# Kernel optimization log

Measured on AMD Instinct MI355X. Metric: run time of the kernel, lower is better.

Reference implementation:

```python
import jax, jax.numpy as jnp
import numpy as np
from jax import lax

# sRGB linear -> LMS matrix (Oklab M1)
M1 = jnp.array([[0.4122214708, 0.5363325363, 0.0514459929],
                [0.2119034982, 0.6806995451, 0.1073969566],
                [0.0883024619, 0.2817188376, 0.6299787005]], dtype=jnp.float32)
# LMS^(1/3) -> Oklab matrix (Oklab M2)
M2 = jnp.array([[0.2104542553, 0.7936177850, -0.0040720468],
                [1.9779984951, -2.4285922050, 0.4505937099],
                [0.0259040371, 0.7827717662, -0.8086757660]], dtype=jnp.float32)
_SX = jnp.array([[-1., 0., 1.], [-2., 0., 2.], [-1., 0., 1.]], dtype=jnp.float32)
_SY = jnp.array([[-1., -2., -1.], [0., 0., 0.], [1., 2., 1.]], dtype=jnp.float32)
SOBEL = jnp.stack([_SX, _SY])[:, None]  # (2,1,3,3) cross-correlation kernels

CLOSING_KERNEL = 11
CLOSING_PAD = CLOSING_KERNEL // 2
EDGE_THRESHOLD = 0.5
POST_DILATION = 2
EPS = 0.01


def _srgb_to_linear(srgb):
    srgb = jnp.clip(srgb, 0.0, 1.0)
    return jnp.where(srgb <= 0.04045, srgb / 12.92, ((srgb + 0.055) / 1.055) ** 2.4)


def _rgb_to_oklab(rgb):  # [B,3,H,W] -> [B,3,H,W]
    linear = _srgb_to_linear(rgb)
    lms = jnp.einsum('oc,bchw->bohw', M1, linear)
    lms = jnp.clip(lms, 1e-10, None) ** (1.0 / 3.0)
    return jnp.einsum('oc,bchw->bohw', M2, lms)


def _max_pool(x, k, p):  # torch max_pool2d pads with -inf implicitly
    return lax.reduce_window(x, -jnp.inf, lax.max, (1, 1, k, k), (1, 1, 1, 1),
                             [(0, 0), (0, 0), (p, p), (p, p)])


def _min_pool(x, k, p):  # -max_pool(-x): padding becomes +inf
    return lax.reduce_window(x, jnp.inf, lax.min, (1, 1, k, k), (1, 1, 1, 1),
                             [(0, 0), (0, 0), (p, p), (p, p)])


def _omni_edge(img):  # [B,C,H,W] -> [B,1,H,W]
    B, C, H, W = img.shape
    flat = img.reshape(B * C, 1, H, W)
    g = lax.conv_general_dilated(flat, SOBEL, (1, 1), [(1, 1), (1, 1)])  # [B*C,2,H,W]
    grad = (jnp.abs(g[:, 0]) + jnp.abs(g[:, 1])).reshape(B, C, H, W)
    return jnp.max(grad, axis=1, keepdims=True)


def _crevice_mask(target):
    edge_soft = jnp.clip(_omni_edge(target) / EDGE_THRESHOLD, 0.0, 1.0)
    dilated = _max_pool(edge_soft, CLOSING_KERNEL, CLOSING_PAD)
    closed = _min_pool(dilated, CLOSING_KERNEL, CLOSING_PAD)
    mask = jax.nn.relu(closed - edge_soft)
    if POST_DILATION > 0:
        dk = 2 * POST_DILATION + 1
        mask = _max_pool(mask, dk, POST_DILATION)
    return mask


def setup_inputs() -> dict:
    key = jax.random.key(0)
    k1, k2 = jax.random.split(key)
    shape = (8, 3, 1024, 1024)
    pred = jax.random.uniform(k1, shape, dtype=jnp.float32)
    target = jax.random.uniform(k2, shape, dtype=jnp.float32)
    return {"pred": pred, "target": target}


def reference(pred, target):
    crevice_mask = _crevice_mask(target)
    mask_sum = jnp.maximum(crevice_mask.sum(), 1.0)
    pred_lab = _rgb_to_oklab(pred)
    target_lab = _rgb_to_oklab(target)
    p_a, p_b = pred_lab[:, 1:2], pred_lab[:, 2:3]
    t_a, t_b = target_lab[:, 1:2], target_lab[:, 2:3]
    C_pred = jnp.sqrt(p_a ** 2 + p_b ** 2 + 1e-12)
    C_gt = jnp.sqrt(t_a ** 2 + t_b ** 2 + 1e-12)
    chroma_loss = (jnp.abs(C_pred - C_gt) * crevice_mask).sum() / mask_sum
    dot_ab = p_a * t_a + p_b * t_b
    cos_hue_diff = jnp.clip(dot_ab / (C_pred * C_gt + 1e-12), -1.0, 1.0)
    hue_loss = (jnp.clip(C_gt, EPS, None) * (1.0 - cos_hue_diff) * crevice_mask).sum() / mask_sum
    return chroma_loss + 2.0 * hue_loss
```

## Files before the change

kernel.cpp:

```cpp
#include <hip/hip_runtime.h>
#include <math.h>

#define SROWS 64
#define PCH   16
#define QCAP  1024


__device__ __forceinline__ float srgb_to_linear(float x) {
    x = fminf(fmaxf(x, 0.0f), 1.0f);
    return (x <= 0.04045f) ? x * (1.0f / 12.92f)
                           : powf((x + 0.055f) * (1.0f / 1.055f), 2.4f);
}

__device__ __forceinline__ void oklab_ab(float r, float g, float b,
                                         float& A, float& Bc) {
    r = srgb_to_linear(r);
    g = srgb_to_linear(g);
    b = srgb_to_linear(b);
    float l = 0.4122214708f * r + 0.5363325363f * g + 0.0514459929f * b;
    float m = 0.2119034982f * r + 0.6806995451f * g + 0.1073969566f * b;
    float s = 0.0883024619f * r + 0.2817188376f * g + 0.6299787005f * b;
    l = cbrtf(fmaxf(l, 1e-10f));
    m = cbrtf(fmaxf(m, 1e-10f));
    s = cbrtf(fmaxf(s, 1e-10f));
    A  = 1.9779984951f * l - 2.428592205f * m + 0.4505937099f * s;
    Bc = 0.0259040371f * l + 0.7827717662f * m - 0.808675766f  * s;
}

__device__ __forceinline__ void color_terms(const float* __restrict__ pred,
                                            const float* __restrict__ target,
                                            size_t off, size_t HWp, float m,
                                            float& sc, float& sh) {
    float pa, pb, ta, tb;
    oklab_ab(pred[off], pred[off + HWp], pred[off + 2 * HWp], pa, pb);
    oklab_ab(target[off], target[off + HWp], target[off + 2 * HWp], ta, tb);
    float Cp = sqrtf(pa * pa + pb * pb + 1e-12f);
    float Cg = sqrtf(ta * ta + tb * tb + 1e-12f);
    sc += fabsf(Cp - Cg) * m;
    float cosd = (pa * ta + pb * tb) / (Cp * Cg + 1e-12f);
    cosd = fminf(fmaxf(cosd, -1.0f), 1.0f);
    sh += fmaxf(Cg, 0.01f) * (1.0f - cosd) * m;
}


__global__ __launch_bounds__(256) void k1_edge(const float* __restrict__ target,
                                               float* __restrict__ edge,
                                               int H, int W) {
    const int WC = 62, BC = 248;
    int cb = (W + BC - 1) / BC;
    int rs = H / SROWS;
    int blk = blockIdx.x;
    int b   = blk / (cb * rs);
    int t   = blk % (cb * rs);
    int bxi = t / rs, ysi = t % rs;
    int lane = threadIdx.x & 63, wid = threadIdx.x >> 6;
    int c  = bxi * BC + wid * WC + lane - 1;
    int y0 = ysi * SROWS;
    size_t plane = (size_t)H * W;
    const float* tb = target + (size_t)b * 3 * plane;
    bool inc = (c >= 0 && c < W);
    bool store_ok = (lane >= 1 && lane <= WC && c < W);
    float* ep = edge + (size_t)b * plane + c;
    int lp = min(lane + 1, 63), lm = max(lane - 1, 0);

    float pr0, pr1, pr2, cu0, cu1, cu2;
    {
        bool ok = inc && (y0 - 1 >= 0);
        const float* p = tb + (size_t)(y0 - 1) * W + c;
        pr0 = ok ? p[0] : 0.f; pr1 = ok ? p[plane] : 0.f; pr2 = ok ? p[2 * plane] : 0.f;
    }
    {
        const float* p = tb + (size_t)y0 * W + c;
        cu0 = inc ? p[0] : 0.f; cu1 = inc ? p[plane] : 0.f; cu2 = inc ? p[2 * plane] : 0.f;
    }
#pragma unroll 2
    for (int y = y0; y < y0 + SROWS; ++y) {
        bool ok = inc && (y + 1 < H);
        const float* p = tb + (size_t)(y + 1) * W + c;
        float nx0 = ok ? p[0] : 0.f;
        float nx1 = ok ? p[plane] : 0.f;
        float nx2 = ok ? p[2 * plane] : 0.f;
        float g = 0.f;
#define SOBEL_CH(PR, CU, NX)                                              \
        {                                                                 \
            float u = PR + 2.f * CU + NX;                                 \
            float v = NX - PR;                                            \
            float up = __shfl(u, lp), um = __shfl(u, lm);                 \
            float vp = __shfl(v, lp), vm = __shfl(v, lm);                 \
            g = fmaxf(g, fabsf(up - um) + fabsf(vm + 2.f * v + vp));      \
        }
        SOBEL_CH(pr0, cu0, nx0)
        SOBEL_CH(pr1, cu1, nx1)
        SOBEL_CH(pr2, cu2, nx2)
#undef SOBEL_CH
        if (store_ok) ep[(size_t)y * W] = fminf(2.f * g, 1.f);
        pr0 = cu0; pr1 = cu1; pr2 = cu2;
        cu0 = nx0; cu1 = nx1; cu2 = nx2;
    }
}


template <int R, bool ISMAX, bool SUB_EDGE>
__global__ __launch_bounds__(256) void pool_kernel(const float* __restrict__ in,
                                                   const float* __restrict__ edge,
                                                   float* __restrict__ out,
                                                   int H, int W) {
    const int OUTW = 256 - 2 * R;
    __shared__ float s_v[PCH][256];
    int cb = (W + OUTW - 1) / OUTW;
    int rs = H / SROWS;
    int blk = blockIdx.x;
    int b   = blk / (cb * rs);
    int t   = blk % (cb * rs);
    int bxi = t / rs, ysi = t % rs;
    int tid = threadIdx.x;
    int col = bxi * OUTW - R + tid;
    int cc  = min(max(col, 0), W - 1);
    size_t base = (size_t)b * H * W;
    const float* colp = in + base + cc;
    int ys = ysi * SROWS;
    bool writer = (tid >= R) && (tid < OUTW + R) && (col < W);

    for (int ph = 0; ph < SROWS / PCH; ++ph) {
        int y0 = ys + ph * PCH;
        float w[PCH + 2 * R];
#pragma unroll
        for (int k = 0; k < PCH + 2 * R; ++k) {
            int r = min(max(y0 - R + k, 0), H - 1);
            w[k] = colp[(size_t)r * W];
        }
        float v[PCH];
#pragma unroll
        for (int k = 0; k < PCH; ++k) {
            float m = w[k];
#pragma unroll
            for (int d = 1; d <= 2 * R; ++d)
                m = ISMAX ? fmaxf(m, w[k + d]) : fminf(m, w[k + d]);
            v[k] = m;
        }
        __syncthreads();
#pragma unroll
        for (int k = 0; k < PCH; ++k) s_v[k][tid] = v[k];
        __syncthreads();
        if (writer) {
#pragma unroll
            for (int k = 0; k < PCH; ++k) {
                float m = s_v[k][tid - R];
#pragma unroll
                for (int d = 1; d <= 2 * R; ++d)
                    m = ISMAX ? fmaxf(m, s_v[k][tid - R + d])
                              : fminf(m, s_v[k][tid - R + d]);
                size_t gi = base + (size_t)(y0 + k) * W + col;
                out[gi] = SUB_EDGE ? fmaxf(m - edge[gi], 0.f) : m;
            }
        }
    }
}


__global__ __launch_bounds__(256) void k4_loss(const float* __restrict__ pred,
                                               const float* __restrict__ target,
                                               const float* __restrict__ mask0,
                                               float* __restrict__ partials,
                                               int H, int W, int nb) {
    const int R = 2, OUTW = 256 - 2 * R;
    __shared__ float s_v[PCH][256];
    __shared__ int   q_pos[QCAP];
    __shared__ float q_m[QCAP];
    __shared__ int   cnt;
    __shared__ float s_red[3][4];

    int cb = (W + OUTW - 1) / OUTW;
    int rs = H / SROWS;
    int blk = blockIdx.x;
    int b   = blk / (cb * rs);
    int t   = blk % (cb * rs);
    int bxi = t / rs, ysi = t % rs;
    int tid = threadIdx.x;
    int col = bxi * OUTW - R + tid;
    int cc  = min(max(col, 0), W - 1);
    size_t HWp  = (size_t)H * W;
    size_t base = (size_t)b * HWp;
    size_t cbase = (size_t)b * 3 * HWp;
    const float* colp = mask0 + base + cc;
    int ys = ysi * SROWS;
    bool writer = (tid >= R) && (tid < OUTW + R) && (col < W);

    float sm = 0.f, sc = 0.f, sh = 0.f;

    for (int ph = 0; ph < SROWS / PCH; ++ph) {
        int y0 = ys + ph * PCH;
        float w[PCH + 2 * R];
#pragma unroll
        for (int k = 0; k < PCH + 2 * R; ++k) {
            int r = min(max(y0 - R + k, 0), H - 1);
            w[k] = colp[(size_t)r * W];
        }
        float v[PCH];
#pragma unroll
        for (int k = 0; k < PCH; ++k) {
            float m = w[k];
#pragma unroll
            for (int d = 1; d <= 2 * R; ++d) m = fmaxf(m, w[k + d]);
            v[k] = m;
        }
        __syncthreads();
#pragma unroll
        for (int k = 0; k < PCH; ++k) s_v[k][tid] = v[k];
        if (tid == 0) cnt = 0;
        __syncthreads();
        if (writer) {
#pragma unroll
            for (int k = 0; k < PCH; ++k) {
                float m = s_v[k][tid - R];
#pragma unroll
                for (int d = 1; d <= 2 * R; ++d)
                    m = fmaxf(m, s_v[k][tid - R + d]);
                sm += m;
                if (m > 0.f) {
                    int pos = atomicAdd(&cnt, 1);
                    if (pos < QCAP) {
                        q_pos[pos] = ((y0 + k) << 16) | col;
                        q_m[pos] = m;
                    } else {
                        color_terms(pred, target,
                                    cbase + (size_t)(y0 + k) * W + col,
                                    HWp, m, sc, sh);
                    }
                }
            }
        }
        __syncthreads();
        int n = min(cnt, QCAP);
        for (int i = tid; i < n; i += 256) {
            int pk = q_pos[i];
            color_terms(pred, target,
                        cbase + (size_t)(pk >> 16) * W + (pk & 0xffff),
                        HWp, q_m[i], sc, sh);
        }
    }

#pragma unroll
    for (int off = 32; off > 0; off >>= 1) {
        sm += __shfl_down(sm, off);
        sc += __shfl_down(sc, off);
        sh += __shfl_down(sh, off);
    }
    int lane = tid & 63, wav = tid >> 6;
    __syncthreads();
    if (lane == 0) { s_red[0][wav] = sm; s_red[1][wav] = sc; s_red[2][wav] = sh; }
    __syncthreads();
    if (tid == 0) {
        float tm = 0, tc = 0, th = 0;
        for (int i = 0; i < 4; ++i) {
            tm += s_red[0][i]; tc += s_red[1][i]; th += s_red[2][i];
        }
        partials[blk]          = tm;
        partials[nb + blk]     = tc;
        partials[2 * nb + blk] = th;
    }
}

__global__ void finalize_kernel(const float* __restrict__ partials, int nb,
                                float* __restrict__ out) {
    double sm = 0.0, sc = 0.0, sh = 0.0;
    for (int i = threadIdx.x; i < nb; i += blockDim.x) {
        sm += (double)partials[i];
        sc += (double)partials[nb + i];
        sh += (double)partials[2 * nb + i];
    }
    __shared__ double red[3][256];
    red[0][threadIdx.x] = sm;
    red[1][threadIdx.x] = sc;
    red[2][threadIdx.x] = sh;
    __syncthreads();
    for (int s = blockDim.x / 2; s > 0; s >>= 1) {
        if ((int)threadIdx.x < s) {
            red[0][threadIdx.x] += red[0][threadIdx.x + s];
            red[1][threadIdx.x] += red[1][threadIdx.x + s];
            red[2][threadIdx.x] += red[2][threadIdx.x + s];
        }
        __syncthreads();
    }
    if (threadIdx.x == 0) {
        double ms = fmax(red[0][0], 1.0);
        out[0] = (float)(red[1][0] / ms + 2.0 * red[2][0] / ms);
    }
}


extern "C" void kernel_launch(void* const* d_in, const int* in_sizes, int n_in,
                              void* d_out, int out_size, void* d_ws, size_t ws_size,
                              hipStream_t stream) {
    const float* pred   = (const float*)d_in[0];
    const float* target = (const float*)d_in[1];
    float* out = (float*)d_out;

    const int H = 1024, W = 1024;
    int Bn = in_sizes[0] / (3 * H * W);
    size_t plane = (size_t)Bn * H * W * sizeof(float);

    char* ws = (char*)d_ws;
    float* planeA = (float*)ws;
    float* planeB = (float*)(ws + plane);
    float* partials = (float*)(ws + 2 * plane);

    int rs = H / SROWS;
    int cb1 = (W + 247) / 248;
    int cbP = (W + 245) / 246;
    int cb4 = (W + 251) / 252;
    int g1 = Bn * cb1 * rs;
    int gP = Bn * cbP * rs;
    int g4 = Bn * cb4 * rs;

    k1_edge<<<g1, 256, 0, stream>>>(target, planeA, H, W);
    pool_kernel<5, true, false><<<gP, 256, 0, stream>>>(planeA, nullptr, planeB, H, W);
    pool_kernel<5, false, true><<<gP, 256, 0, stream>>>(planeB, planeA, planeA, H, W);
    k4_loss<<<g4, 256, 0, stream>>>(pred, target, planeA, partials, H, W, g4);
    finalize_kernel<<<1, 256, 0, stream>>>(partials, g4, out);
}
```

Baseline: 109.7 us.

## Fuse Sobel edge kernel with 11x11 max-pool dilation into one kernel

Merges the edge-detection kernel and the first max-pool pass into a single kernel that computes Sobel edges for 16-row chunks plus a 5-row halo, then does vertical and horizontal max-dilation through shared memory. It writes both the edge plane and the dilated plane, removing one full-plane write/read round trip and a kernel launch. In exchange it recomputes edges in halo rows and columns, which adds redundant Sobel work, uses more shared memory and registers (a 28-value window per thread), and adds extra barriers per chunk.

New measurement: 266.2 us. 2.43x slower.

```diff
diff --git a/kernel.cpp b/kernel.cpp
--- a/kernel.cpp
+++ b/kernel.cpp
@@ -4,6 +4,7 @@
 #define SROWS 64
 #define PCH   16
 #define QCAP  1024
+#define OUTW12 244
 
 
 __device__ __forceinline__ float srgb_to_linear(float x) {
@@ -43,59 +44,117 @@
 }
 
 
-__global__ __launch_bounds__(256) void k1_edge(const float* __restrict__ target,
-                                               float* __restrict__ edge,
-                                               int H, int W) {
-    const int WC = 62, BC = 248;
-    int cb = (W + BC - 1) / BC;
-    int rs = H / SROWS;
+__global__ __launch_bounds__(256) void k12_fused(const float* __restrict__ target,
+                                                 float* __restrict__ edge,
+                                                 float* __restrict__ dil,
+                                                 int H, int W) {
+    __shared__ float s_u[26][256];
+    __shared__ float s_v[26][256];
+    float (*s_dv)[256] = s_u;
+
+    int cgs = (W + OUTW12 - 1) / OUTW12;
+    int rs  = H / SROWS;
     int blk = blockIdx.x;
-    int b   = blk / (cb * rs);
-    int t   = blk % (cb * rs);
-    int bxi = t / rs, ysi = t % rs;
-    int lane = threadIdx.x & 63, wid = threadIdx.x >> 6;
-    int c  = bxi * BC + wid * WC + lane - 1;
-    int y0 = ysi * SROWS;
-    size_t plane = (size_t)H * W;
-    const float* tb = target + (size_t)b * 3 * plane;
-    bool inc = (c >= 0 && c < W);
-    bool store_ok = (lane >= 1 && lane <= WC && c < W);
-    float* ep = edge + (size_t)b * plane + c;
-    int lp = min(lane + 1, 63), lm = max(lane - 1, 0);
-
-    float pr0, pr1, pr2, cu0, cu1, cu2;
-    {
-        bool ok = inc && (y0 - 1 >= 0);
-        const float* p = tb + (size_t)(y0 - 1) * W + c;
-        pr0 = ok ? p[0] : 0.f; pr1 = ok ? p[plane] : 0.f; pr2 = ok ? p[2 * plane] : 0.f;
-    }
-    {
-        const float* p = tb + (size_t)y0 * W + c;
-        cu0 = inc ? p[0] : 0.f; cu1 = inc ? p[plane] : 0.f; cu2 = inc ? p[2 * plane] : 0.f;
-    }
-#pragma unroll 2
-    for (int y = y0; y < y0 + SROWS; ++y) {
-        bool ok = inc && (y + 1 < H);
-        const float* p = tb + (size_t)(y + 1) * W + c;
-        float nx0 = ok ? p[0] : 0.f;
-        float nx1 = ok ? p[plane] : 0.f;
-        float nx2 = ok ? p[2 * plane] : 0.f;
-        float g = 0.f;
-#define SOBEL_CH(PR, CU, NX)                                              \
-        {                                                                 \
-            float u = PR + 2.f * CU + NX;                                 \
-            float v = NX - PR;                                            \
-            float up = __shfl(u, lp), um = __shfl(u, lm);                 \
-            float vp = __shfl(v, lp), vm = __shfl(v, lm);                 \
-            g = fmaxf(g, fabsf(up - um) + fabsf(vm + 2.f * v + vp));      \
-        }
-        SOBEL_CH(pr0, cu0, nx0)
-        SOBEL_CH(pr1, cu1, nx1)
-        SOBEL_CH(pr2, cu2, nx2)
-#undef SOBEL_CH
-        if (store_ok) ep[(size_t)y * W] = fminf(2.f * g, 1.f);
-        pr0 = cu0; pr1 = cu1; pr2 = cu2;
-        cu0 = nx0; cu1 = nx1; cu2 = nx2;
+    int b   = blk / (cgs * rs);
+    int rem = blk % (cgs * rs);
+    int bxi = rem / rs, ysi = rem % rs;
+    int t   = threadIdx.x;
+    int c0  = bxi * OUTW12;
+    int gcol = c0 - 6 + t;
+    int scc  = min(max(gcol, 0), W - 1);
+    bool colok = (gcol >= 0) && (gcol < W);
+    size_t HW = (size_t)H * W;
+    const float* tb = target + (size_t)b * 3 * HW + scc;
+    size_t obase = (size_t)b * HW;
+    int ys = ysi * SROWS;
+    int tl = max(t - 1, 0), tr = min(t + 1, 255);
+
+    int gc2 = min(max(gcol, 0), W - 1);
+    int tc  = gc2 - (c0 - 6);
+    bool needfix = (gcol != gc2);
+
+    bool dil_store  = (t < OUTW12) && (c0 + t < W);
+    bool edge_store = (t >= 6) && (t < 6 + OUTW12) && (gcol < W);
+
+    for (int ph = 0; ph < SROWS / PCH; ++ph) {
+        int f0 = ys + ph * PCH;
+        float e[26];
+#pragma unroll
+        for (int i = 0; i < 26; ++i) e[i] = 0.f;
+
+        for (int c = 0; c < 3; ++c) {
+            const float* p = tb + (size_t)c * HW;
+            float w[28];
+#pragma unroll
+            for (int i = 0; i < 28; ++i) {
+                int r  = f0 - 6 + i;
+                int rc = min(max(r, 0), H - 1);
+                float val = p[(size_t)rc * W];
+                w[i] = (colok && r >= 0 && r < H) ? val : 0.f;
+            }
+            float u[26], v[26];
+#pragma unroll
+            for (int i = 0; i < 26; ++i) {
+                u[i] = fmaf(2.f, w[i + 1], w[i]) + w[i + 2];
+                v[i] = w[i + 2] - w[i];
+            }
+            __syncthreads();
+#pragma unroll
+            for (int i = 0; i < 26; ++i) {
+                s_u[i][t] = u[i];
+                s_v[i][t] = v[i];
+            }
+            __syncthreads();
+#pragma unroll
+            for (int i = 0; i < 26; ++i) {
+                float ul = s_u[i][tl], ur = s_u[i][tr];
+                float vl = s_v[i][tl], vr = s_v[i][tr];
+                float gx = ur - ul;
+                float gy = fmaf(2.f, v[i], vl) + vr;
+                e[i] = fmaxf(e[i], fabsf(gx) + fabsf(gy));
+            }
+        }
+#pragma unroll
+        for (int i = 0; i < 26; ++i) e[i] = fminf(2.f * e[i], 1.f);
+        if (f0 == 0) {
+            e[0] = e[5]; e[1] = e[5]; e[2] = e[5]; e[3] = e[5]; e[4] = e[5];
+        }
+        if (f0 == H - PCH) {
+            e[21] = e[20]; e[22] = e[20]; e[23] = e[20]; e[24] = e[20];
+            e[25] = e[20];
+        }
+        float dv[16];
+#pragma unroll
+        for (int m = 0; m < 16; m += 2) {
+            float M = e[m + 1];
+#pragma unroll
+            for (int d = 2; d <= 10; ++d) M = fmaxf(M, e[m + d]);
+            dv[m]     = fmaxf(M, e[m]);
+            dv[m + 1] = fmaxf(M, e[m + 11]);
+        }
+        __syncthreads();
+#pragma unroll
+        for (int k = 0; k < 16; ++k) s_dv[k][t] = dv[k];
+        __syncthreads();
+        if (needfix) {
+#pragma unroll
+            for (int k = 0; k < 16; ++k) s_dv[k][t] = s_dv[k][tc];
+        }
+        __syncthreads();
+        if (dil_store) {
+#pragma unroll
+            for (int k = 0; k < 16; ++k) {
+                float m = s_dv[k][t + 1];
+#pragma unroll
+                for (int d = 2; d <= 11; ++d) m = fmaxf(m, s_dv[k][t + d]);
+                dil[obase + (size_t)(f0 + k) * W + (c0 + t)] = m;
+            }
+        }
+        if (edge_store) {
+#pragma unroll
+            for (int k = 0; k < 16; ++k)
+                edge[obase + (size_t)(f0 + k) * W + gcol] = e[5 + k];
+        }
     }
 }
 
@@ -251,12 +310,12 @@
     if (lane == 0) { s_red[0][wav] = sm; s_red[1][wav] = sc; s_red[2][wav] = sh; }
     __syncthreads();
     if (tid == 0) {
-        float tm = 0, tc = 0, th = 0;
+        float tm = 0, tc2 = 0, th = 0;
         for (int i = 0; i < 4; ++i) {
-            tm += s_red[0][i]; tc += s_red[1][i]; th += s_red[2][i];
+            tm += s_red[0][i]; tc2 += s_red[1][i]; th += s_red[2][i];
         }
         partials[blk]          = tm;
-        partials[nb + blk]     = tc;
+        partials[nb + blk]     = tc2;
         partials[2 * nb + blk] = th;
     }
 }
@@ -305,16 +364,15 @@
     float* planeB = (float*)(ws + plane);
     float* partials = (float*)(ws + 2 * plane);
 
-    int rs = H / SROWS;
-    int cb1 = (W + 247) / 248;
+    int rs  = H / SROWS;
+    int cgs = (W + OUTW12 - 1) / OUTW12;
+    int g12 = Bn * cgs * rs;
     int cbP = (W + 245) / 246;
     int cb4 = (W + 251) / 252;
-    int g1 = Bn * cb1 * rs;
     int gP = Bn * cbP * rs;
     int g4 = Bn * cb4 * rs;
 
-    k1_edge<<<g1, 256, 0, stream>>>(target, planeA, H, W);
-    pool_kernel<5, true, false><<<gP, 256, 0, stream>>>(planeA, nullptr, planeB, H, W);
+    k12_fused<<<g12, 256, 0, stream>>>(target, planeA, planeB, H, W);
     pool_kernel<5, false, true><<<gP, 256, 0, stream>>>(planeB, planeA, planeA, H, W);
     k4_loss<<<g4, 256, 0, stream>>>(pred, target, planeA, partials, H, W, g4);
     finalize_kernel<<<1, 256, 0, stream>>>(partials, g4, out);
```

## Rewrite Sobel edge kernel with LDS row chunks instead of wavefront shuffles

Applied to the files above, without the earlier changes.

The edge kernel changes from per-wavefront column strips with a rolling three-row register window and lane shuffles to 256-wide block tiles. Each thread loads 18 rows per channel into registers and stages vertical partial sums in shared memory so neighbours can read them. This removes the four shuffles per channel per row and the 2-lane halo loss per wavefront (254 useful columns per 256 instead of 248), and issues many independent loads at once. The cost is two block barriers per channel chunk, two re-read halo rows per 16-row chunk, and a change in grid shape to 32-row strips.

Result: slower. 145.6 us (+32.7%).

```diff
diff --git a/kernel.cpp b/kernel.cpp
--- a/kernel.cpp
+++ b/kernel.cpp
@@ -4,6 +4,9 @@
 #define SROWS 64
 #define PCH   16
 #define QCAP  1024
+#define K1_PCH  16
+#define K1_SROWS 32
+#define K1_OUTW 254
 
 
 __device__ __forceinline__ float srgb_to_linear(float x) {
@@ -46,56 +49,63 @@
 __global__ __launch_bounds__(256) void k1_edge(const float* __restrict__ target,
                                                float* __restrict__ edge,
                                                int H, int W) {
-    const int WC = 62, BC = 248;
-    int cb = (W + BC - 1) / BC;
-    int rs = H / SROWS;
+    __shared__ float s_u[K1_PCH][256];
+    __shared__ float s_v[K1_PCH][256];
+
+    int cb  = (W + K1_OUTW - 1) / K1_OUTW;
+    int rs  = H / K1_SROWS;
     int blk = blockIdx.x;
     int b   = blk / (cb * rs);
-    int t   = blk % (cb * rs);
-    int bxi = t / rs, ysi = t % rs;
-    int lane = threadIdx.x & 63, wid = threadIdx.x >> 6;
-    int c  = bxi * BC + wid * WC + lane - 1;
-    int y0 = ysi * SROWS;
-    size_t plane = (size_t)H * W;
-    const float* tb = target + (size_t)b * 3 * plane;
-    bool inc = (c >= 0 && c < W);
-    bool store_ok = (lane >= 1 && lane <= WC && c < W);
-    float* ep = edge + (size_t)b * plane + c;
-    int lp = min(lane + 1, 63), lm = max(lane - 1, 0);
-
-    float pr0, pr1, pr2, cu0, cu1, cu2;
-    {
-        bool ok = inc && (y0 - 1 >= 0);
-        const float* p = tb + (size_t)(y0 - 1) * W + c;
-        pr0 = ok ? p[0] : 0.f; pr1 = ok ? p[plane] : 0.f; pr2 = ok ? p[2 * plane] : 0.f;
-    }
-    {
-        const float* p = tb + (size_t)y0 * W + c;
-        cu0 = inc ? p[0] : 0.f; cu1 = inc ? p[plane] : 0.f; cu2 = inc ? p[2 * plane] : 0.f;
-    }
-#pragma unroll 2
-    for (int y = y0; y < y0 + SROWS; ++y) {
-        bool ok = inc && (y + 1 < H);
-        const float* p = tb + (size_t)(y + 1) * W + c;
-        float nx0 = ok ? p[0] : 0.f;
-        float nx1 = ok ? p[plane] : 0.f;
-        float nx2 = ok ? p[2 * plane] : 0.f;
-        float g = 0.f;
-#define SOBEL_CH(PR, CU, NX)                                              \
-        {                                                                 \
-            float u = PR + 2.f * CU + NX;                                 \
-            float v = NX - PR;                                            \
-            float up = __shfl(u, lp), um = __shfl(u, lm);                 \
-            float vp = __shfl(v, lp), vm = __shfl(v, lm);                 \
-            g = fmaxf(g, fabsf(up - um) + fabsf(vm + 2.f * v + vp));      \
-        }
-        SOBEL_CH(pr0, cu0, nx0)
-        SOBEL_CH(pr1, cu1, nx1)
-        SOBEL_CH(pr2, cu2, nx2)
-#undef SOBEL_CH
-        if (store_ok) ep[(size_t)y * W] = fminf(2.f * g, 1.f);
-        pr0 = cu0; pr1 = cu1; pr2 = cu2;
-        cu0 = nx0; cu1 = nx1; cu2 = nx2;
+    int rem = blk % (cb * rs);
+    int bxi = rem / rs, ysi = rem % rs;
+    int t   = threadIdx.x;
+    int c0  = bxi * K1_OUTW;
+    int gcol = c0 - 1 + t;
+    int scc  = min(max(gcol, 0), W - 1);
+    bool colok = (gcol >= 0) && (gcol < W);
+    size_t HW = (size_t)H * W;
+    const float* tb = target + (size_t)b * 3 * HW + scc;
+    float* ep = edge + (size_t)b * HW;
+    int ys = ysi * K1_SROWS;
+    bool writer = (t >= 1) && (t < 1 + K1_OUTW) && (gcol < W);
+    int tl = max(t - 1, 0), tr = min(t + 1, 255);
+
+    for (int ph = 0; ph < K1_SROWS / K1_PCH; ++ph) {
+        int f0 = ys + ph * K1_PCH;
+        float e[K1_PCH];
+#pragma unroll
+        for (int i = 0; i < K1_PCH; ++i) e[i] = 0.f;
+
+        for (int c = 0; c < 3; ++c) {
+            const float* p = tb + (size_t)c * HW;
+            float w[K1_PCH + 2];
+#pragma unroll
+            for (int i = 0; i < K1_PCH + 2; ++i) {
+                int r  = f0 - 1 + i;
+                int rc = min(max(r, 0), H - 1);
+                float val = p[(size_t)rc * W];
+                w[i] = (colok && r >= 0 && r < H) ? val : 0.f;
+            }
+            __syncthreads();
+#pragma unroll
+            for (int i = 0; i < K1_PCH; ++i) {
+                s_u[i][t] = fmaf(2.f, w[i + 1], w[i]) + w[i + 2];
+                s_v[i][t] = w[i + 2] - w[i];
+            }
+            __syncthreads();
+#pragma unroll
+            for (int i = 0; i < K1_PCH; ++i) {
+                float vc = w[i + 2] - w[i];
+                float gx = s_u[i][tr] - s_u[i][tl];
+                float gy = fmaf(2.f, vc, s_v[i][tl]) + s_v[i][tr];
+                e[i] = fmaxf(e[i], fabsf(gx) + fabsf(gy));
+            }
+        }
+        if (writer) {
+#pragma unroll
+            for (int i = 0; i < K1_PCH; ++i)
+                ep[(size_t)(f0 + i) * W + gcol] = fminf(2.f * e[i], 1.f);
+        }
     }
 }
 
@@ -305,11 +315,12 @@
     float* planeB = (float*)(ws + plane);
     float* partials = (float*)(ws + 2 * plane);
 
-    int rs = H / SROWS;
-    int cb1 = (W + 247) / 248;
+    int rs1 = H / K1_SROWS;
+    int cb1 = (W + K1_OUTW - 1) / K1_OUTW;
+    int g1  = Bn * cb1 * rs1;
+    int rs  = H / SROWS;
     int cbP = (W + 245) / 246;
     int cb4 = (W + 251) / 252;
-    int g1 = Bn * cb1 * rs;
     int gP = Bn * cbP * rs;
     int g4 = Bn * cb4 * rs;
 
```
